# Optimization experiments

Measured on AMD Instinct MI355X. Metric: run time of the kernel, lower is better.

The kernel has to match this reference:

```python
import jax, jax.numpy as jnp
import numpy as np

N = 50000
E = 600000
IN_C = 128
HID = 128
OUT_C = 2


def setup_inputs() -> dict:
    key = jax.random.key(0)
    ks = jax.random.split(key, 16)
    x = jax.random.normal(ks[0], (N, IN_C), dtype=jnp.float32)
    edge_index = jax.random.randint(ks[1], (2, E), 0, N, dtype=jnp.int64)
    s = 0.05
    # policy_net: Linear(2*in, 64) -> ReLU -> Linear(64, 1) -> Sigmoid
    W_p1 = jax.random.normal(ks[2], (64, 2 * IN_C), dtype=jnp.float32) * s
    b_p1 = jnp.zeros((64,), dtype=jnp.float32)
    W_p2 = jax.random.normal(ks[3], (1, 64), dtype=jnp.float32) * s
    b_p2 = jnp.zeros((1,), dtype=jnp.float32)
    # GCNConv weights (lin without bias + separate bias, PyG convention)
    W1 = jax.random.normal(ks[4], (HID, IN_C), dtype=jnp.float32) * s
    b1 = jnp.zeros((HID,), dtype=jnp.float32)
    W2 = jax.random.normal(ks[5], (HID, HID), dtype=jnp.float32) * s
    b2 = jnp.zeros((HID,), dtype=jnp.float32)
    W_lin = jax.random.normal(ks[6], (OUT_C, HID), dtype=jnp.float32) * s
    b_lin = jnp.zeros((OUT_C,), dtype=jnp.float32)
    return {"x": x, "edge_index": edge_index, "W_p1": W_p1, "b_p1": b_p1,
            "W_p2": W_p2, "b_p2": b_p2, "W1": W1, "b1": b1, "W2": W2,
            "b2": b2, "W_lin": W_lin, "b_lin": b_lin}


def gcn_conv(x, src, dst, edge_weight, W, b, n_nodes):
    # PyG GCNConv with normalize=True, add_self_loops=True, given edge_weight.
    loop = jnp.arange(n_nodes, dtype=src.dtype)
    s = jnp.concatenate([src, loop])
    d = jnp.concatenate([dst, loop])
    w = jnp.concatenate([edge_weight, jnp.ones((n_nodes,), x.dtype)])
    deg = jax.ops.segment_sum(w, d, num_segments=n_nodes)
    dinv = jnp.where(deg > 0, jax.lax.rsqrt(jnp.where(deg > 0, deg, 1.0)), 0.0)
    norm = dinv[s] * w * dinv[d]  # [E+N]
    xl = x @ W.T  # [N, out]
    msg = norm[:, None] * xl[s]  # gather + scale
    agg = jax.ops.segment_sum(msg, d, num_segments=n_nodes)
    return agg + b


def reference(x, edge_index, W_p1, b_p1, W_p2, b_p2, W1, b1, W2, b2, W_lin, b_lin):
    src, dst = edge_index[0], edge_index[1]
    # edge-weight policy MLP on gathered, concatenated endpoint features
    cat_feat = jnp.concatenate([x[src], x[dst]], axis=1)  # [E, 2*in]
    h = jax.nn.relu(cat_feat @ W_p1.T + b_p1)
    edge_weight = jax.nn.sigmoid(h @ W_p2.T + b_p2)[:, 0]  # [E]
    x1 = jax.nn.relu(gcn_conv(x, src, dst, edge_weight, W1, b1, N))
    x2 = jax.nn.relu(gcn_conv(x1, src, dst, edge_weight, W2, b2, N))
    out = x2 @ W_lin.T + b_lin
    return jax.nn.sigmoid(out)
```

## Files before the change

### kernel.cpp

```cpp
#include <hip/hip_runtime.h>
#include <hip/hip_bf16.h>

#define NN 50000
#define NE 600000
#define CPAD 16

typedef __attribute__((ext_vector_type(8))) short short8;
typedef __attribute__((ext_vector_type(8))) _Float16 half8;
typedef __attribute__((ext_vector_type(4))) float floatx4;

__device__ __forceinline__ short bf16_bits(float v) {
    __hip_bfloat16 h = __float2bfloat16(v);
    return *reinterpret_cast<short*>(&h);
}

__device__ __forceinline__ void stage_w(const short* __restrict__ src, short* lds) {
    int t = threadIdx.x;
#pragma unroll
    for (int i = 0; i < 8; ++i) {
        int gci = t + i * 256;
        int row = gci >> 4, ci = gci & 15;
        short8 v = *(const short8*)(src + gci * 8);
        *(short8*)(lds + row * 128 + ((ci ^ (row & 7)) << 3)) = v;
    }
}

__global__ void k_init_cvt(const int* __restrict__ raw, int* __restrict__ count,
                           int* __restrict__ flag, const float* __restrict__ wp1,
                           const float* __restrict__ w1, const float* __restrict__ w2,
                           __hip_bfloat16* __restrict__ wcatb, __hip_bfloat16* __restrict__ w1b,
                           __hip_bfloat16* __restrict__ w2b) {
    int i = blockIdx.x * blockDim.x + threadIdx.x;
    if (i < NN) {
        count[(size_t)i * CPAD] = 0;
    }
    if (i < 16384) {
        int r = i >> 7, c = i & 127;
        float v = (r < 64) ? wp1[r * 256 + c] : wp1[(r - 64) * 256 + 128 + c];
        wcatb[i] = __float2bfloat16(v);
    } else if (i < 32768) {
        w1b[i - 16384] = __float2bfloat16(w1[i - 16384]);
    } else if (i < 49152) {
        w2b[i - 32768] = __float2bfloat16(w2[i - 32768]);
    }
    if (blockIdx.x == 0) {
        if (threadIdx.x == 0) *flag = 0;
        __syncthreads();
        int any = 0;
        for (int j = threadIdx.x; j < 1024; j += 256) any |= raw[2 * j + 1];
        if (any) atomicOr(flag, 1);
    }
}

#define GCNT 293
#define GG 782
__global__ __launch_bounds__(256) void k_uv_cnt(
    const float* __restrict__ x, const __hip_bfloat16* __restrict__ Wb,
    const float* __restrict__ bp1, _Float16* __restrict__ uvh,
    __hip_bfloat16* __restrict__ xb, const int* __restrict__ raw,
    const int* __restrict__ flag, int* __restrict__ count, int* __restrict__ rank) {
    if (blockIdx.x < GCNT) {
        const bool f32 = (*flag) != 0;
        const long long* r64 = (const long long*)raw;
        int gid = blockIdx.x * 256 + threadIdx.x;
        int e0 = gid * 8;
        if (e0 + 8 <= NE) {
            int dd[8];
            if (f32) {
#pragma unroll
                for (int k = 0; k < 8; ++k) dd[k] = raw[NE + e0 + k];
            } else {
#pragma unroll
                for (int k = 0; k < 8; ++k) dd[k] = (int)r64[NE + e0 + k];
            }
            int rk[8];
#pragma unroll
            for (int k = 0; k < 8; ++k) rk[k] = atomicAdd(&count[(size_t)dd[k] * CPAD], 1);
#pragma unroll
            for (int k = 0; k < 8; ++k) rank[e0 + k] = rk[k];
        } else {
            for (int e = e0; e < NE; ++e) {
                int d = f32 ? raw[NE + e] : (int)r64[NE + e];
                rank[e] = atomicAdd(&count[(size_t)d * CPAD], 1);
            }
        }
        return;
    }
    __shared__ short wlds[16384];
    stage_w((const short*)Wb, wlds);
    __syncthreads();

    const int lane = threadIdx.x & 63;
    const int wave = threadIdx.x >> 6;
    const int col = lane & 15;
    const int quad = lane >> 4;

    int tile = (blockIdx.x - GCNT) * 4 + wave;
    if (tile >= NN / 16) return;
    int base = tile * 16;

    short8 bfrag[4][8];
    const int rx = col & 7;
#pragma unroll
    for (int tt = 0; tt < 8; ++tt) {
        int row = tt * 16 + col;
#pragma unroll
        for (int kk = 0; kk < 4; ++kk)
            bfrag[kk][tt] = *(const short8*)(wlds + row * 128 + (((kk * 4 + quad) ^ rx) << 3));
    }

    floatx4 acc[8];
#pragma unroll
    for (int t = 0; t < 8; ++t) acc[t] = (floatx4){0.f, 0.f, 0.f, 0.f};
#pragma unroll
    for (int kk = 0; kk < 4; ++kk) {
        const float* xrow = x + (size_t)(base + col) * 128 + kk * 32 + quad * 8;
        float4 f0 = ((const float4*)xrow)[0];
        float4 f1 = ((const float4*)xrow)[1];
        short8 afrag;
        afrag[0] = bf16_bits(f0.x); afrag[1] = bf16_bits(f0.y);
        afrag[2] = bf16_bits(f0.z); afrag[3] = bf16_bits(f0.w);
        afrag[4] = bf16_bits(f1.x); afrag[5] = bf16_bits(f1.y);
        afrag[6] = bf16_bits(f1.z); afrag[7] = bf16_bits(f1.w);
        *(short8*)((short*)xb + (size_t)(base + col) * 128 + kk * 32 + quad * 8) = afrag;
#pragma unroll
        for (int tt = 0; tt < 8; ++tt)
            acc[tt] = __builtin_amdgcn_mfma_f32_16x16x32_bf16(afrag, bfrag[kk][tt], acc[tt], 0, 0, 0);
    }
#pragma unroll
    for (int tt = 0; tt < 8; ++tt) {
        int n = tt * 16 + col;
        float badd = (tt >= 4) ? bp1[n - 64] : 0.f;
#pragma unroll
        for (int r = 0; r < 4; ++r) {
            int row = base + quad * 4 + r;
            uvh[(size_t)row * 128 + n] = (_Float16)(acc[tt][r] + badd);
        }
    }
}

__global__ void k_scan_block(const int* __restrict__ count, int* __restrict__ tmp,
                             int* __restrict__ bsums) {
    __shared__ int s[512];
    int tid = threadIdx.x;
    int i = blockIdx.x * 512 + tid;
    s[tid] = (i < NN) ? count[(size_t)i * CPAD] : 0;
    __syncthreads();
    for (int off = 1; off < 512; off <<= 1) {
        int t = (tid >= off) ? s[tid - off] : 0;
        __syncthreads();
        s[tid] += t;
        __syncthreads();
    }
    if (i < NN) tmp[i] = s[tid];
    if (tid == 511) bsums[blockIdx.x] = s[511];
}

#define GFIN 196
#define GPOL 9375
__global__ __launch_bounds__(256) void k_fin_policy(
    const int* __restrict__ tmp, const int* __restrict__ bsums, int* __restrict__ rowptr,
    const int* __restrict__ raw, const int* __restrict__ flag,
    const _Float16* __restrict__ uvh, const float* __restrict__ wp2,
    const float* __restrict__ bp2, float* __restrict__ ew_flat) {
    if (blockIdx.x < GFIN) {
        __shared__ int sb[128];
        int tid = threadIdx.x;
        if (tid < 128) sb[tid] = (tid < 98) ? bsums[tid] : 0;
        __syncthreads();
        for (int off = 1; off < 128; off <<= 1) {
            int t = (tid < 128 && tid >= off) ? sb[tid - off] : 0;
            __syncthreads();
            if (tid < 128) sb[tid] += t;
            __syncthreads();
        }
        int i = blockIdx.x * 256 + tid;
        if (i >= NN) return;
        int blk = i >> 9;
        int add = blk ? sb[blk - 1] : 0;
        rowptr[i + 1] = tmp[i] + add;
        if (i == 0) rowptr[0] = 0;
        return;
    }
    const bool f32 = (*flag) != 0;
    const long long* r64 = (const long long*)raw;
    int pb = blockIdx.x - GFIN;
    int wave = threadIdx.x >> 6, lane = threadIdx.x & 63;
    int g = lane >> 3, c = lane & 7;
    int e1 = pb * 64 + wave * 16 + g;
    int e2 = e1 + 8;
    int s1, d1, s2, d2;
    if (f32) {
        s1 = raw[e1]; d1 = raw[NE + e1];
        s2 = raw[e2]; d2 = raw[NE + e2];
    } else {
        s1 = (int)r64[e1]; d1 = (int)r64[NE + e1];
        s2 = (int)r64[e2]; d2 = (int)r64[NE + e2];
    }
    half8 u1 = *(const half8*)(uvh + (size_t)s1 * 128 + c * 8);
    half8 v1 = *(const half8*)(uvh + (size_t)d1 * 128 + 64 + c * 8);
    half8 u2 = *(const half8*)(uvh + (size_t)s2 * 128 + c * 8);
    half8 v2 = *(const half8*)(uvh + (size_t)d2 * 128 + 64 + c * 8);
    float w2v[8];
    const float4* w2p = (const float4*)(wp2 + c * 8);
    float4 wa = w2p[0], wb = w2p[1];
    w2v[0] = wa.x; w2v[1] = wa.y; w2v[2] = wa.z; w2v[3] = wa.w;
    w2v[4] = wb.x; w2v[5] = wb.y; w2v[6] = wb.z; w2v[7] = wb.w;
    float b2 = bp2[0];
    float p1 = 0.f, p2 = 0.f;
#pragma unroll
    for (int j = 0; j < 8; ++j) {
        float h1 = (float)u1[j] + (float)v1[j];
        float h2 = (float)u2[j] + (float)v2[j];
        h1 = h1 > 0.f ? h1 : 0.f;
        h2 = h2 > 0.f ? h2 : 0.f;
        p1 += h1 * w2v[j];
        p2 += h2 * w2v[j];
    }
    p1 += __shfl_xor(p1, 1, 64); p2 += __shfl_xor(p2, 1, 64);
    p1 += __shfl_xor(p1, 2, 64); p2 += __shfl_xor(p2, 2, 64);
    p1 += __shfl_xor(p1, 4, 64); p2 += __shfl_xor(p2, 4, 64);
    if (c == 0) {
        ew_flat[e1] = 1.f / (1.f + __expf(-(p1 + b2)));
        ew_flat[e2] = 1.f / (1.f + __expf(-(p2 + b2)));
    }
}

__global__ void k_fill(const int* __restrict__ raw, const int* __restrict__ flag,
                       const int* __restrict__ rank, const int* __restrict__ rowptr,
                       const float* __restrict__ ew_flat, int2* __restrict__ meta) {
    int t = blockIdx.x * blockDim.x + threadIdx.x;
    int e0 = t * 4;
    if (e0 >= NE) return;
    const bool f32 = (*flag) != 0;
    const long long* r64 = (const long long*)raw;
    int s[4], d[4], rk[4];
    float ew[4];
#pragma unroll
    for (int k = 0; k < 4; ++k) {
        int e = e0 + k;
        if (f32) { s[k] = raw[e]; d[k] = raw[NE + e]; }
        else     { s[k] = (int)r64[e]; d[k] = (int)r64[NE + e]; }
        rk[k] = rank[e];
        ew[k] = ew_flat[e];
    }
    int base[4];
#pragma unroll
    for (int k = 0; k < 4; ++k) base[k] = rowptr[d[k]];
#pragma unroll
    for (int k = 0; k < 4; ++k) meta[base[k] + rk[k]] = make_int2(s[k], __float_as_int(ew[k]));
}

template <bool CDEG>
__global__ __launch_bounds__(256) void k_gemm(
    const __hip_bfloat16* __restrict__ A, const __hip_bfloat16* __restrict__ Wb,
    const int* __restrict__ rowptr, const int2* __restrict__ meta,
    float* __restrict__ deg, _Float16* __restrict__ xlh) {
    __shared__ short wlds[16384];
    stage_w((const short*)Wb, wlds);
    __syncthreads();

    const int lane = threadIdx.x & 63;
    const int wave = threadIdx.x >> 6;
    const int col = lane & 15;
    const int quad = lane >> 4;

    int tile = blockIdx.x * 4 + wave;
    if (tile >= NN / 16) return;
    int base = tile * 16;

    short8 bfrag[4][8];
    const int rx = col & 7;
#pragma unroll
    for (int tt = 0; tt < 8; ++tt) {
        int row = tt * 16 + col;
#pragma unroll
        for (int kk = 0; kk < 4; ++kk)
            bfrag[kk][tt] = *(const short8*)(wlds + row * 128 + (((kk * 4 + quad) ^ rx) << 3));
    }
    const short* xs = (const short*)A;

    floatx4 acc[8];
#pragma unroll
    for (int t = 0; t < 8; ++t) acc[t] = (floatx4){0.f, 0.f, 0.f, 0.f};
#pragma unroll
    for (int kk = 0; kk < 4; ++kk) {
        short8 afrag = *(const short8*)(xs + (size_t)(base + col) * 128 + kk * 32 + quad * 8);
#pragma unroll
        for (int tt = 0; tt < 8; ++tt)
            acc[tt] = __builtin_amdgcn_mfma_f32_16x16x32_bf16(afrag, bfrag[kk][tt], acc[tt], 0, 0, 0);
    }
    float di[4];
    if (CDEG) {
        int rn = base + col;
        int beg = rowptr[rn], end = rowptr[rn + 1];
        float sdeg = 0.f;
        for (int p = beg + quad; p < end; p += 4) sdeg += __int_as_float(meta[p].y);
        sdeg += __shfl_xor(sdeg, 16, 64);
        sdeg += __shfl_xor(sdeg, 32, 64);
        float dv = 1.f + sdeg;
        if (quad == 0) deg[rn] = dv;
#pragma unroll
        for (int r = 0; r < 4; ++r) di[r] = rsqrtf(__shfl(dv, quad * 4 + r, 64));
    } else {
#pragma unroll
        for (int r = 0; r < 4; ++r) di[r] = rsqrtf(deg[base + quad * 4 + r]);
    }
#pragma unroll
    for (int tt = 0; tt < 8; ++tt) {
        int n = tt * 16 + col;
#pragma unroll
        for (int r = 0; r < 4; ++r) {
            int row = base + quad * 4 + r;
            xlh[(size_t)row * 128 + n] = (_Float16)(di[r] * acc[tt][r]);
        }
    }
}

__device__ __forceinline__ void scatter_core(
    const int* __restrict__ rowptr, const int2* __restrict__ meta,
    const _Float16* __restrict__ xlh, int wid, int g, int c, float acc[8]) {
    int beg = rowptr[wid], end = rowptr[wid + 1];
    int p = beg + g;
    for (; p + 12 < end; p += 16) {
        int2 m1 = meta[p], m2 = meta[p + 4], m3 = meta[p + 8], m4 = meta[p + 12];
        half8 r1 = *(const half8*)(xlh + (size_t)m1.x * 128 + c * 8);
        half8 r2 = *(const half8*)(xlh + (size_t)m2.x * 128 + c * 8);
        half8 r3 = *(const half8*)(xlh + (size_t)m3.x * 128 + c * 8);
        half8 r4 = *(const half8*)(xlh + (size_t)m4.x * 128 + c * 8);
        float c1 = __int_as_float(m1.y), c2 = __int_as_float(m2.y);
        float c3 = __int_as_float(m3.y), c4 = __int_as_float(m4.y);
#pragma unroll
        for (int j = 0; j < 8; ++j)
            acc[j] += c1 * (float)r1[j] + c2 * (float)r2[j] + c3 * (float)r3[j] + c4 * (float)r4[j];
    }
    for (; p + 4 < end; p += 8) {
        int2 m1 = meta[p], m2 = meta[p + 4];
        half8 r1 = *(const half8*)(xlh + (size_t)m1.x * 128 + c * 8);
        half8 r2 = *(const half8*)(xlh + (size_t)m2.x * 128 + c * 8);
        float c1 = __int_as_float(m1.y), c2 = __int_as_float(m2.y);
#pragma unroll
        for (int j = 0; j < 8; ++j) acc[j] += c1 * (float)r1[j] + c2 * (float)r2[j];
    }
    if (p < end) {
        int2 m1 = meta[p];
        half8 r1 = *(const half8*)(xlh + (size_t)m1.x * 128 + c * 8);
        float c1 = __int_as_float(m1.y);
#pragma unroll
        for (int j = 0; j < 8; ++j) acc[j] += c1 * (float)r1[j];
    }
#pragma unroll
    for (int j = 0; j < 8; ++j) {
        acc[j] += __shfl_xor(acc[j], 16, 64);
        acc[j] += __shfl_xor(acc[j], 32, 64);
    }
}

__global__ __launch_bounds__(256) void k_scatter_mid(
    const int* __restrict__ rowptr, const int2* __restrict__ meta,
    const float* __restrict__ deg, const _Float16* __restrict__ xlh,
    const float* __restrict__ bias, __hip_bfloat16* __restrict__ xb2) {
    int wid = (blockIdx.x * blockDim.x + threadIdx.x) >> 6;
    int lane = threadIdx.x & 63;
    if (wid >= NN) return;
    int g = lane >> 4, c = lane & 15;
    float acc[8] = {0.f, 0.f, 0.f, 0.f, 0.f, 0.f, 0.f, 0.f};
    scatter_core(rowptr, meta, xlh, wid, g, c, acc);
    if (g == 0) {
        float dn = rsqrtf(deg[wid]);
        half8 sv = *(const half8*)(xlh + (size_t)wid * 128 + c * 8);
        const float4* bp = (const float4*)(bias + c * 8);
        float4 ba = bp[0], bb = bp[1];
        float bv[8] = {ba.x, ba.y, ba.z, ba.w, bb.x, bb.y, bb.z, bb.w};
        short8 o;
#pragma unroll
        for (int j = 0; j < 8; ++j) {
            float t = bv[j] + dn * ((float)sv[j] + acc[j]);
            t = t > 0.f ? t : 0.f;
            o[j] = bf16_bits(t);
        }
        *(short8*)((short*)xb2 + (size_t)wid * 128 + c * 8) = o;
    }
}

__global__ __launch_bounds__(256) void k_scatter_out(
    const int* __restrict__ rowptr, const int2* __restrict__ meta,
    const float* __restrict__ deg, const _Float16* __restrict__ xlh,
    const float* __restrict__ bias, const float* __restrict__ wlin,
    const float* __restrict__ blin, float* __restrict__ out) {
    int wid = (blockIdx.x * blockDim.x + threadIdx.x) >> 6;
    int lane = threadIdx.x & 63;
    if (wid >= NN) return;
    int g = lane >> 4, c = lane & 15;
    float acc[8] = {0.f, 0.f, 0.f, 0.f, 0.f, 0.f, 0.f, 0.f};
    scatter_core(rowptr, meta, xlh, wid, g, c, acc);
    if (g == 0) {
        float dn = rsqrtf(deg[wid]);
        half8 sv = *(const half8*)(xlh + (size_t)wid * 128 + c * 8);
        const float4* bp = (const float4*)(bias + c * 8);
        float4 ba = bp[0], bb = bp[1];
        float bv[8] = {ba.x, ba.y, ba.z, ba.w, bb.x, bb.y, bb.z, bb.w};
        float p0 = 0.f, p1 = 0.f;
#pragma unroll
        for (int j = 0; j < 8; ++j) {
            float t = bv[j] + dn * ((float)sv[j] + acc[j]);
            t = t > 0.f ? t : 0.f;
            p0 += t * wlin[c * 8 + j];
            p1 += t * wlin[128 + c * 8 + j];
        }
#pragma unroll
        for (int off = 1; off < 16; off <<= 1) {
            p0 += __shfl_xor(p0, off, 64);
            p1 += __shfl_xor(p1, off, 64);
        }
        if (c == 0) {
            out[wid * 2 + 0] = 1.f / (1.f + __expf(-(p0 + blin[0])));
            out[wid * 2 + 1] = 1.f / (1.f + __expf(-(p1 + blin[1])));
        }
    }
}


extern "C" void kernel_launch(void* const* d_in, const int* in_sizes, int n_in,
                              void* d_out, int out_size, void* d_ws, size_t ws_size,
                              hipStream_t stream) {
    const float* x = (const float*)d_in[0];
    const int* eidx_raw = (const int*)d_in[1];
    const float* W_p1 = (const float*)d_in[2];
    const float* b_p1 = (const float*)d_in[3];
    const float* W_p2 = (const float*)d_in[4];
    const float* b_p2 = (const float*)d_in[5];
    const float* W1 = (const float*)d_in[6];
    const float* b1 = (const float*)d_in[7];
    const float* W2 = (const float*)d_in[8];
    const float* b2 = (const float*)d_in[9];
    const float* W_lin = (const float*)d_in[10];
    const float* b_lin = (const float*)d_in[11];
    float* out = (float*)d_out;

    char* ws = (char*)d_ws;
    size_t off = 0;
    auto alloc = [&](size_t bytes) -> void* {
        off = (off + 255) & ~(size_t)255;
        void* p = ws + off;
        off += bytes;
        return p;
    };
    float* deg = (float*)alloc(NN * 4);
    int* rowptr = (int*)alloc((NN + 1) * 4);
    int* count = (int*)alloc((size_t)NN * CPAD * 4);
    int* flag = (int*)alloc(4);
    int* bsums = (int*)alloc(128 * 4);
    int* rank = (int*)alloc((size_t)NE * 4);
    float* ew_flat = (float*)alloc((size_t)NE * 4);
    int2* meta = (int2*)alloc((size_t)NE * 8);
    __hip_bfloat16* xb = (__hip_bfloat16*)alloc((size_t)NN * 128 * 2);
    _Float16* xlh = (_Float16*)alloc((size_t)NN * 128 * 2);
    _Float16* uvh = (_Float16*)alloc((size_t)NN * 128 * 2);
    __hip_bfloat16* wcatb = (__hip_bfloat16*)alloc(128 * 128 * 2);
    __hip_bfloat16* w1b = (__hip_bfloat16*)alloc(128 * 128 * 2);
    __hip_bfloat16* w2b = (__hip_bfloat16*)alloc(128 * 128 * 2);
    int* tmp = (int*)meta;

    const int TB = 256;
    int gN = (NN + TB - 1) / TB;
    int gF = (NE / 4 + TB - 1) / TB;
    int gS = (NN + 3) / 4;

    k_init_cvt<<<gN, TB, 0, stream>>>(eidx_raw, count, flag, W_p1, W1, W2, wcatb, w1b, w2b);
    k_uv_cnt<<<GCNT + GG, TB, 0, stream>>>(x, wcatb, b_p1, uvh, xb, eidx_raw, flag, count, rank);
    k_scan_block<<<98, 512, 0, stream>>>(count, tmp, bsums);
    k_fin_policy<<<GFIN + GPOL, TB, 0, stream>>>(tmp, bsums, rowptr, eidx_raw, flag, uvh,
                                                 W_p2, b_p2, ew_flat);
    k_fill<<<gF, TB, 0, stream>>>(eidx_raw, flag, rank, rowptr, ew_flat, meta);
    k_gemm<true><<<GG, TB, 0, stream>>>(xb, w1b, rowptr, meta, deg, xlh);
    k_scatter_mid<<<gS, TB, 0, stream>>>(rowptr, meta, deg, xlh, b1, xb);
    k_gemm<false><<<GG, TB, 0, stream>>>(xb, w2b, rowptr, meta, deg, xlh);
    k_scatter_out<<<gS, TB, 0, stream>>>(rowptr, meta, deg, xlh, b2, W_lin, b_lin, out);
}
```

Measured before the change: 237.2 us.

## Fuse scan finalization via decoupled lookback and merge policy with CSR fill

Replaces the two-pass prefix scan (block scan plus a separate finalize stage) with a single kernel in which each block publishes its sum through an atomic flag and spin-waits on its predecessors' sums to build rowptr. The edge policy MLP kernel now writes directly into the CSR meta array using rank and rowptr, which removes the ew_flat intermediate and the separate fill kernel. This cuts two launches and one round-trip of edge-weight data through global memory. The lookback spin relies on all 98 blocks being co-resident to avoid deadlock, and the fused fill issues scattered writes from only one lane per eight.

```diff
diff --git a/kernel.cpp b/kernel.cpp
--- a/kernel.cpp
+++ b/kernel.cpp
@@ -26,7 +26,8 @@
 }
 
 __global__ void k_init_cvt(const int* __restrict__ raw, int* __restrict__ count,
-                           int* __restrict__ flag, const float* __restrict__ wp1,
+                           int* __restrict__ flag, int* __restrict__ bsums,
+                           const float* __restrict__ wp1,
                            const float* __restrict__ w1, const float* __restrict__ w2,
                            __hip_bfloat16* __restrict__ wcatb, __hip_bfloat16* __restrict__ w1b,
                            __hip_bfloat16* __restrict__ w2b) {
@@ -34,6 +35,7 @@
     if (i < NN) {
         count[(size_t)i * CPAD] = 0;
     }
+    if (i < 128) bsums[i] = 0;
     if (i < 16384) {
         int r = i >> 7, c = i & 127;
         float v = (r < 64) ? wp1[r * 256 + c] : wp1[(r - 64) * 256 + 128 + c];
@@ -139,11 +141,12 @@
     }
 }
 
-__global__ void k_scan_block(const int* __restrict__ count, int* __restrict__ tmp,
-                             int* __restrict__ bsums) {
+__global__ __launch_bounds__(512) void k_scan_rowptr(
+    const int* __restrict__ count, int* __restrict__ bsums, int* __restrict__ rowptr) {
     __shared__ int s[512];
-    int tid = threadIdx.x;
-    int i = blockIdx.x * 512 + tid;
+    __shared__ int red[512];
+    int tid = threadIdx.x, bid = blockIdx.x;
+    int i = bid * 512 + tid;
     s[tid] = (i < NN) ? count[(size_t)i * CPAD] : 0;
     __syncthreads();
     for (int off = 1; off < 512; off <<= 1) {
@@ -152,39 +155,33 @@
         s[tid] += t;
         __syncthreads();
     }
-    if (i < NN) tmp[i] = s[tid];
-    if (tid == 511) bsums[blockIdx.x] = s[511];
-}
-
-#define GFIN 196
+    if (tid == 511) atomicExch(&bsums[bid], s[511] + 1);
+    int part = 0;
+    for (int j = tid; j < bid; j += 512) {
+        int v;
+        do { v = atomicAdd(&bsums[j], 0); } while (v == 0);
+        part += v - 1;
+    }
+    red[tid] = part;
+    __syncthreads();
+    for (int off = 256; off > 0; off >>= 1) {
+        if (tid < off) red[tid] += red[tid + off];
+        __syncthreads();
+    }
+    int prefix = red[0];
+    if (i < NN) rowptr[i + 1] = s[tid] + prefix;
+    if (bid == 0 && tid == 0) rowptr[0] = 0;
+}
+
 #define GPOL 9375
-__global__ __launch_bounds__(256) void k_fin_policy(
-    const int* __restrict__ tmp, const int* __restrict__ bsums, int* __restrict__ rowptr,
+__global__ __launch_bounds__(256) void k_pol_fill(
     const int* __restrict__ raw, const int* __restrict__ flag,
+    const int* __restrict__ rank, const int* __restrict__ rowptr,
     const _Float16* __restrict__ uvh, const float* __restrict__ wp2,
-    const float* __restrict__ bp2, float* __restrict__ ew_flat) {
-    if (blockIdx.x < GFIN) {
-        __shared__ int sb[128];
-        int tid = threadIdx.x;
-        if (tid < 128) sb[tid] = (tid < 98) ? bsums[tid] : 0;
-        __syncthreads();
-        for (int off = 1; off < 128; off <<= 1) {
-            int t = (tid < 128 && tid >= off) ? sb[tid - off] : 0;
-            __syncthreads();
-            if (tid < 128) sb[tid] += t;
-            __syncthreads();
-        }
-        int i = blockIdx.x * 256 + tid;
-        if (i >= NN) return;
-        int blk = i >> 9;
-        int add = blk ? sb[blk - 1] : 0;
-        rowptr[i + 1] = tmp[i] + add;
-        if (i == 0) rowptr[0] = 0;
-        return;
-    }
+    const float* __restrict__ bp2, int2* __restrict__ meta) {
     const bool f32 = (*flag) != 0;
     const long long* r64 = (const long long*)raw;
-    int pb = blockIdx.x - GFIN;
+    int pb = blockIdx.x;
     int wave = threadIdx.x >> 6, lane = threadIdx.x & 63;
     int g = lane >> 3, c = lane & 7;
     int e1 = pb * 64 + wave * 16 + g;
@@ -221,34 +218,13 @@
     p1 += __shfl_xor(p1, 2, 64); p2 += __shfl_xor(p2, 2, 64);
     p1 += __shfl_xor(p1, 4, 64); p2 += __shfl_xor(p2, 4, 64);
     if (c == 0) {
-        ew_flat[e1] = 1.f / (1.f + __expf(-(p1 + b2)));
-        ew_flat[e2] = 1.f / (1.f + __expf(-(p2 + b2)));
-    }
-}
-
-__global__ void k_fill(const int* __restrict__ raw, const int* __restrict__ flag,
-                       const int* __restrict__ rank, const int* __restrict__ rowptr,
-                       const float* __restrict__ ew_flat, int2* __restrict__ meta) {
-    int t = blockIdx.x * blockDim.x + threadIdx.x;
-    int e0 = t * 4;
-    if (e0 >= NE) return;
-    const bool f32 = (*flag) != 0;
-    const long long* r64 = (const long long*)raw;
-    int s[4], d[4], rk[4];
-    float ew[4];
-#pragma unroll
-    for (int k = 0; k < 4; ++k) {
-        int e = e0 + k;
-        if (f32) { s[k] = raw[e]; d[k] = raw[NE + e]; }
-        else     { s[k] = (int)r64[e]; d[k] = (int)r64[NE + e]; }
-        rk[k] = rank[e];
-        ew[k] = ew_flat[e];
-    }
-    int base[4];
-#pragma unroll
-    for (int k = 0; k < 4; ++k) base[k] = rowptr[d[k]];
-#pragma unroll
-    for (int k = 0; k < 4; ++k) meta[base[k] + rk[k]] = make_int2(s[k], __float_as_int(ew[k]));
+        float ew1 = 1.f / (1.f + __expf(-(p1 + b2)));
+        float ew2 = 1.f / (1.f + __expf(-(p2 + b2)));
+        int rk1 = rank[e1], rk2 = rank[e2];
+        int rb1 = rowptr[d1], rb2 = rowptr[d2];
+        meta[rb1 + rk1] = make_int2(s1, __float_as_int(ew1));
+        meta[rb2 + rk2] = make_int2(s2, __float_as_int(ew2));
+    }
 }
 
 template <bool CDEG>
@@ -452,7 +428,6 @@
     int* flag = (int*)alloc(4);
     int* bsums = (int*)alloc(128 * 4);
     int* rank = (int*)alloc((size_t)NE * 4);
-    float* ew_flat = (float*)alloc((size_t)NE * 4);
     int2* meta = (int2*)alloc((size_t)NE * 8);
     __hip_bfloat16* xb = (__hip_bfloat16*)alloc((size_t)NN * 128 * 2);
     _Float16* xlh = (_Float16*)alloc((size_t)NN * 128 * 2);
@@ -460,19 +435,15 @@
     __hip_bfloat16* wcatb = (__hip_bfloat16*)alloc(128 * 128 * 2);
     __hip_bfloat16* w1b = (__hip_bfloat16*)alloc(128 * 128 * 2);
     __hip_bfloat16* w2b = (__hip_bfloat16*)alloc(128 * 128 * 2);
-    int* tmp = (int*)meta;
 
     const int TB = 256;
     int gN = (NN + TB - 1) / TB;
-    int gF = (NE / 4 + TB - 1) / TB;
     int gS = (NN + 3) / 4;
 
-    k_init_cvt<<<gN, TB, 0, stream>>>(eidx_raw, count, flag, W_p1, W1, W2, wcatb, w1b, w2b);
+    k_init_cvt<<<gN, TB, 0, stream>>>(eidx_raw, count, flag, bsums, W_p1, W1, W2, wcatb, w1b, w2b);
     k_uv_cnt<<<GCNT + GG, TB, 0, stream>>>(x, wcatb, b_p1, uvh, xb, eidx_raw, flag, count, rank);
-    k_scan_block<<<98, 512, 0, stream>>>(count, tmp, bsums);
-    k_fin_policy<<<GFIN + GPOL, TB, 0, stream>>>(tmp, bsums, rowptr, eidx_raw, flag, uvh,
-                                                 W_p2, b_p2, ew_flat);
-    k_fill<<<gF, TB, 0, stream>>>(eidx_raw, flag, rank, rowptr, ew_flat, meta);
+    k_scan_rowptr<<<98, 512, 0, stream>>>(count, bsums, rowptr);
+    k_pol_fill<<<GPOL, TB, 0, stream>>>(eidx_raw, flag, rank, rowptr, uvh, W_p2, b_p2, meta);
     k_gemm<true><<<GG, TB, 0, stream>>>(xb, w1b, rowptr, meta, deg, xlh);
     k_scatter_mid<<<gS, TB, 0, stream>>>(rowptr, meta, deg, xlh, b1, xb);
     k_gemm<false><<<GG, TB, 0, stream>>>(xb, w2b, rowptr, meta, deg, xlh);
```

Measured after the change: 239.0 us. Within noise of the previous version (+0.8%).
